# Optimization experiments

Measured on AMD Instinct MI355X. Metric: run time of the kernel, lower is better.

The kernel has to match this reference:

```python
import jax, jax.numpy as jnp
import numpy as np

N = 50000      # nodes
E = 800000     # edges
F_IN = 128     # infeatures
H = 64         # hidden_channels
NID = 1
MSG_EPS = 1e-7  # GENConv message eps


def layer_norm(x, g, b):
    mu = jnp.mean(x, axis=-1, keepdims=True)
    var = jnp.var(x, axis=-1, keepdims=True)
    return (x - mu) * jax.lax.rsqrt(var + 1e-5) * g + b


def gen_conv(x, src, dst, t, W1, b1, g1, be1, W2, b2):
    # message: relu(x_j) + eps, gathered along edges
    m = jax.nn.relu(x[src]) + MSG_EPS                      # [E, C]
    # softmax aggregation over incoming edges per destination node, per channel
    logits = m * t                                         # [E, C]
    seg_max = jax.ops.segment_max(logits, dst, num_segments=N)
    seg_max = jnp.where(jnp.isfinite(seg_max), seg_max, 0.0)  # isolated nodes
    ex = jnp.exp(logits - seg_max[dst])                    # [E, C]
    denom = jax.ops.segment_sum(ex, dst, num_segments=N)   # [N, C]
    alpha = ex / (denom[dst] + 1e-16)                      # softmax weights per edge
    agg = jax.ops.segment_sum(m * alpha, dst, num_segments=N)  # [N, C]
    out = agg + x                                          # add root
    # MLP: Linear(C->2C) -> LayerNorm -> ReLU -> Linear(2C->C)
    h = jax.nn.relu(layer_norm(out @ W1 + b1, g1, be1))
    return h @ W2 + b2


def setup_inputs() -> dict:
    key = jax.random.key(0)
    ks = jax.random.split(key, 12)
    s = 0.05
    return {
        "x": jax.random.normal(ks[0], (N, F_IN), dtype=jnp.float32),
        "edge_index": jax.random.randint(ks[1], (2, E), 0, N, dtype=jnp.int64),
        "enc_W": jax.random.normal(ks[2], (F_IN, H), dtype=jnp.float32) * s,
        "enc_b": jnp.zeros((H,), jnp.float32),
        "t": jnp.float32(1.0),
        "conv_W1": jax.random.normal(ks[3], (H, 2 * H), dtype=jnp.float32) * s,
        "conv_b1": jnp.zeros((2 * H,), jnp.float32),
        "conv_g1": jnp.ones((2 * H,), jnp.float32),
        "conv_be1": jnp.zeros((2 * H,), jnp.float32),
        "conv_W2": jax.random.normal(ks[4], (2 * H, H), dtype=jnp.float32) * s,
        "conv_b2": jnp.zeros((H,), jnp.float32),
        "ln1_g": jnp.ones((H,), jnp.float32),
        "ln1_b": jnp.zeros((H,), jnp.float32),
        "norm_g": jnp.ones((2 * H,), jnp.float32),
        "norm_b": jnp.zeros((2 * H,), jnp.float32),
        "lin_W": jax.random.normal(ks[5], (2 * H, NID), dtype=jnp.float32) * s,
        "lin_b": jnp.zeros((NID,), jnp.float32),
    }


def reference(x, edge_index, enc_W, enc_b, t, conv_W1, conv_b1, conv_g1, conv_be1,
              conv_W2, conv_b2, ln1_g, ln1_b, norm_g, norm_b, lin_W, lin_b):
    src, dst = edge_index[0], edge_index[1]
    x = x @ enc_W + enc_b                                   # node encoder [N, H]
    # pre-applied conv (layers[0].conv called standalone in original forward)
    x = gen_conv(x, src, dst, t, conv_W1, conv_b1, conv_g1, conv_be1, conv_W2, conv_b2)
    # DeepGCNLayer block='dense' (same conv module, shared weights)
    h = gen_conv(x, src, dst, t, conv_W1, conv_b1, conv_g1, conv_be1, conv_W2, conv_b2)
    h = jax.nn.relu(layer_norm(h, ln1_g, ln1_b))
    x = jnp.concatenate([x, h], axis=-1)                    # [N, 2H] (dropout eval = identity)
    x = jax.nn.relu(layer_norm(x, norm_g, norm_b))
    return x @ lin_W + lin_b                                # [N, NID]
```

## Files before the change

kernel.cpp:

```cpp
#include <hip/hip_runtime.h>
#include <hip/hip_bf16.h>


#define NN 50000
#define EE 800000
#define FIN 128
#define HD 64
#define NBUCK 196
#define CAP 4608
#define EPB 2048
#define NBLK 391

typedef unsigned short u16;
typedef unsigned int u32;
using bf16x8 = __attribute__((ext_vector_type(8))) short;
using f32x4 = __attribute__((ext_vector_type(4))) float;

__device__ __forceinline__ float bf2f(u16 u) {
    u32 x = ((u32)u) << 16;
    float f;
    __builtin_memcpy(&f, &x, 4);
    return f;
}
__device__ __forceinline__ short f2bf(float f) {
    u32 u;
    __builtin_memcpy(&u, &f, 4);
    u32 r = (u + 0x7fffu + ((u >> 16) & 1u)) >> 16;
    return (short)r;
}

__global__ __launch_bounds__(256) void k_detect(const int* __restrict__ ei,
                                                int* __restrict__ flag,
                                                int* __restrict__ bcnt) {
    __shared__ int red[256];
    int t = threadIdx.x;
    int any = 0;
#pragma unroll
    for (int k = 0; k < 4; k++) any |= (ei[2 * (t * 4 + k) + 1] != 0) ? 1 : 0;
    red[t] = any;
    __syncthreads();
    for (int d = 128; d >= 1; d >>= 1) {
        if (t < d) red[t] |= red[t + d];
        __syncthreads();
    }
    if (t == 0) *flag = red[0];
    if (t < NBUCK) bcnt[t] = 0;
}

__global__ __launch_bounds__(256) void k_bucket_enc(
    const int* __restrict__ ei, const int* __restrict__ flag, int* __restrict__ bcnt,
    u32* __restrict__ barr, const float* __restrict__ x, const float* __restrict__ W,
    const float* __restrict__ b, u16* __restrict__ Abf) {
    __shared__ short wtE[64 * 136];
    int tid = threadIdx.x;
    if (blockIdx.x < NBLK) {
        __shared__ int hist[NBUCK];
        __shared__ int gbase[NBUCK];
        __shared__ int cur[NBUCK];
        for (int i = tid; i < NBUCK; i += 256) { hist[i] = 0; cur[i] = 0; }
        __syncthreads();
        int is32 = *flag;
        int e0 = blockIdx.x * EPB;
        u32 pk[8];
#pragma unroll
        for (int j = 0; j < 8; j++) {
            int e = e0 + j * 256 + tid;
            if (e < EE) {
                int s, d;
                if (is32) {
                    s = ei[e];
                    d = ei[EE + e];
                } else {
                    int2 sp = ((const int2*)ei)[e];
                    int2 dp = ((const int2*)ei)[EE + e];
                    s = sp.x;
                    d = dp.x;
                }
                pk[j] = (u32)s | ((u32)(d & 255) << 16) | ((u32)(d >> 8) << 24);
                atomicAdd(&hist[d >> 8], 1);
            } else {
                pk[j] = 0xFFFFFFFFu;
            }
        }
        __syncthreads();
        for (int i = tid; i < NBUCK; i += 256)
            if (hist[i] > 0) gbase[i] = atomicAdd(&bcnt[i], hist[i]);
        __syncthreads();
#pragma unroll
        for (int j = 0; j < 8; j++) {
            if (pk[j] != 0xFFFFFFFFu) {
                int bk = pk[j] >> 24;
                int pos = gbase[bk] + atomicAdd(&cur[bk], 1);
                if (pos < CAP) barr[(size_t)bk * CAP + pos] = pk[j] & 0x00FFFFFFu;
            }
        }
        return;
    }
    for (int i = tid; i < FIN * HD; i += 256) wtE[(i & 63) * 136 + (i >> 6)] = f2bf(W[i]);
    __syncthreads();

    int lane = tid & 63, wid = tid >> 6;
    int l16 = lane & 15, q = lane >> 4;
    int m0 = (int)(blockIdx.x - NBLK) * 64 + wid * 16;
    int mrow = m0 + l16;
    if (mrow >= NN) mrow = NN - 1;

    bf16x8 af[4];
#pragma unroll
    for (int c = 0; c < 4; c++) {
        const float4* p = (const float4*)(x + (size_t)mrow * FIN + c * 32 + q * 8);
        float4 p0 = p[0], p1 = p[1];
        af[c][0] = f2bf(p0.x); af[c][1] = f2bf(p0.y); af[c][2] = f2bf(p0.z); af[c][3] = f2bf(p0.w);
        af[c][4] = f2bf(p1.x); af[c][5] = f2bf(p1.y); af[c][6] = f2bf(p1.z); af[c][7] = f2bf(p1.w);
    }
    f32x4 acc[4];
#pragma unroll
    for (int u = 0; u < 4; u++) {
        f32x4 z = {0.f, 0.f, 0.f, 0.f};
#pragma unroll
        for (int c = 0; c < 4; c++) {
            bf16x8 wf = *(const bf16x8*)(const void*)&wtE[(u * 16 + l16) * 136 + c * 32 + q * 8];
            z = __builtin_amdgcn_mfma_f32_16x16x32_bf16(af[c], wf, z, 0, 0, 0);
        }
        acc[u] = z;
    }
#pragma unroll
    for (int u = 0; u < 4; u++) {
        int col = u * 16 + l16;
        float bc = b[col];
#pragma unroll
        for (int r = 0; r < 4; r++) {
            int node = m0 + q * 4 + r;
            if (node < NN) Abf[(size_t)node * HD + col] = (u16)f2bf(acc[u][r] + bc);
        }
    }
}

__global__ __launch_bounds__(256) void k_sort(const int* __restrict__ bcnt,
                                              const u32* __restrict__ barr,
                                              u16* __restrict__ eSrc,
                                              int* __restrict__ rowLo,
                                              int* __restrict__ deg) {
    __shared__ u32 pkL[CAP];
    __shared__ u16 outL[CAP];
    __shared__ int hist[256];
    __shared__ int excl[256];
    __shared__ int cur[256];
    int bk = blockIdx.x;
    int t = threadIdx.x;
    int cnt = bcnt[bk];
    if (cnt > CAP) cnt = CAP;
    const u32* bp = barr + (size_t)bk * CAP;
    for (int i = t; i < cnt; i += 256) pkL[i] = bp[i];
    hist[t] = 0;
    __syncthreads();
    for (int i = t; i < cnt; i += 256) atomicAdd(&hist[(pkL[i] >> 16) & 0xFF], 1);
    __syncthreads();
    int v = hist[t];
    excl[t] = v;
    __syncthreads();
#pragma unroll
    for (int d = 1; d < 256; d <<= 1) {
        int u = (t >= d) ? excl[t - d] : 0;
        __syncthreads();
        excl[t] += u;
        __syncthreads();
    }
    int ex = excl[t] - v;
    cur[t] = ex;
    int node = bk * 256 + t;
    if (node < NN) {
        rowLo[node] = bk * CAP + ex;
        deg[node] = v;
    }
    __syncthreads();
    for (int i = t; i < cnt; i += 256) {
        u32 pk = pkL[i];
        int pos = atomicAdd(&cur[(pk >> 16) & 0xFF], 1);
        outL[pos] = (u16)pk;
    }
    __syncthreads();
    int cnt2 = (cnt + 1) >> 1;
    u32* dst = (u32*)(void*)(eSrc + (size_t)bk * CAP);
    const u32* src = (const u32*)(const void*)outL;
    for (int i = t; i < cnt2; i += 256) dst[i] = src[i];
}

__global__ __launch_bounds__(256) void k_agg(const u16* __restrict__ Xbf,
                                             const float* __restrict__ Xfp,
                                             const int* __restrict__ rowLo,
                                             const int* __restrict__ deg,
                                             const u16* __restrict__ eSrc,
                                             const float* __restrict__ tptr,
                                             u16* __restrict__ OUTbf) {
    int t = threadIdx.x;
    int lane = t & 63, wid = t >> 6;
    int half = lane >> 5, cp = lane & 31;
    float tt = tptr[0];
    for (int n = blockIdx.x * 4 + wid; n < NN; n += gridDim.x * 4) {
        int s = rowLo[n];
        int e = s + deg[n];
        float self0, self1;
        if (Xfp) {
            float2 f2 = *(const float2*)(Xfp + (size_t)n * HD + 2 * cp);
            self0 = f2.x; self1 = f2.y;
        } else {
            u32 u = *(const u32*)(const void*)(Xbf + (size_t)n * HD + 2 * cp);
            self0 = bf2f((u16)u); self1 = bf2f((u16)(u >> 16));
        }
        float num0 = 0.f, den0 = 0.f, num1 = 0.f, den1 = 0.f;
        int base = s;
        for (; base + 16 <= e; base += 16) {
            int sv[8];
#pragma unroll
            for (int k = 0; k < 8; k++) sv[k] = eSrc[base + 2 * k + half];
            u32 uu[8];
#pragma unroll
            for (int k = 0; k < 8; k++)
                uu[k] = *(const u32*)(const void*)(Xbf + (size_t)sv[k] * HD + 2 * cp);
#pragma unroll
            for (int k = 0; k < 8; k++) {
                float m0 = fmaxf(bf2f((u16)uu[k]), 0.f) + 1e-7f;
                float m1 = fmaxf(bf2f((u16)(uu[k] >> 16)), 0.f) + 1e-7f;
                float p0 = __expf(m0 * tt);
                float p1 = __expf(m1 * tt);
                den0 += p0; num0 += m0 * p0;
                den1 += p1; num1 += m1 * p1;
            }
        }
        if (base + 8 <= e) {
            int sv[4];
#pragma unroll
            for (int k = 0; k < 4; k++) sv[k] = eSrc[base + 2 * k + half];
            u32 uu[4];
#pragma unroll
            for (int k = 0; k < 4; k++)
                uu[k] = *(const u32*)(const void*)(Xbf + (size_t)sv[k] * HD + 2 * cp);
#pragma unroll
            for (int k = 0; k < 4; k++) {
                float m0 = fmaxf(bf2f((u16)uu[k]), 0.f) + 1e-7f;
                float m1 = fmaxf(bf2f((u16)(uu[k] >> 16)), 0.f) + 1e-7f;
                float p0 = __expf(m0 * tt);
                float p1 = __expf(m1 * tt);
                den0 += p0; num0 += m0 * p0;
                den1 += p1; num1 += m1 * p1;
            }
            base += 8;
        }
        int i = base + half;
        for (; i + 2 < e; i += 4) {
            int sva = eSrc[i], svb = eSrc[i + 2];
            u32 ua = *(const u32*)(const void*)(Xbf + (size_t)sva * HD + 2 * cp);
            u32 ub = *(const u32*)(const void*)(Xbf + (size_t)svb * HD + 2 * cp);
            float m0a = fmaxf(bf2f((u16)ua), 0.f) + 1e-7f;
            float m1a = fmaxf(bf2f((u16)(ua >> 16)), 0.f) + 1e-7f;
            float m0b = fmaxf(bf2f((u16)ub), 0.f) + 1e-7f;
            float m1b = fmaxf(bf2f((u16)(ub >> 16)), 0.f) + 1e-7f;
            float p0a = __expf(m0a * tt), p1a = __expf(m1a * tt);
            float p0b = __expf(m0b * tt), p1b = __expf(m1b * tt);
            den0 += p0a + p0b; num0 += m0a * p0a + m0b * p0b;
            den1 += p1a + p1b; num1 += m1a * p1a + m1b * p1b;
        }
        if (i < e) {
            int sv = eSrc[i];
            u32 u = *(const u32*)(const void*)(Xbf + (size_t)sv * HD + 2 * cp);
            float m0 = fmaxf(bf2f((u16)u), 0.f) + 1e-7f;
            float m1 = fmaxf(bf2f((u16)(u >> 16)), 0.f) + 1e-7f;
            float p0 = __expf(m0 * tt);
            float p1 = __expf(m1 * tt);
            den0 += p0; num0 += m0 * p0;
            den1 += p1; num1 += m1 * p1;
        }
        num0 += __shfl_xor(num0, 32, 64);
        den0 += __shfl_xor(den0, 32, 64);
        num1 += __shfl_xor(num1, 32, 64);
        den1 += __shfl_xor(den1, 32, 64);
        if (half == 0) {
            float a0 = num0 / (den0 + 1e-16f) + self0;
            float a1 = num1 / (den1 + 1e-16f) + self1;
            u32 pk = (u32)(u16)f2bf(a0) | ((u32)(u16)f2bf(a1) << 16);
            *(u32*)(void*)(OUTbf + (size_t)n * HD + 2 * cp) = pk;
        }
    }
}

__global__ __launch_bounds__(256) void k_mlp(const u16* __restrict__ INbf,
                                             const float* __restrict__ W1,
                                             const float* __restrict__ B1,
                                             const float* __restrict__ G1,
                                             const float* __restrict__ BE1,
                                             const float* __restrict__ W2,
                                             const float* __restrict__ B2,
                                             float* __restrict__ OUTfp,
                                             u16* __restrict__ OUTbf) {
    __shared__ short wt1[128 * 72];
    __shared__ short wt2[64 * 136];
    __shared__ short hbuf[64 * 136];
    int tid = threadIdx.x;
    for (int i = tid; i < HD * 128; i += 256) wt1[(i & 127) * 72 + (i >> 7)] = f2bf(W1[i]);
    for (int i = tid; i < 128 * HD; i += 256) wt2[(i & 63) * 136 + (i >> 6)] = f2bf(W2[i]);
    __syncthreads();

    int lane = tid & 63, wid = tid >> 6;
    int l16 = lane & 15, q = lane >> 4;
    int m0 = blockIdx.x * 64 + wid * 16;
    int mrow = m0 + l16;
    if (mrow >= NN) mrow = NN - 1;

    float b1v[8], g1v[8], bev[8];
#pragma unroll
    for (int tl = 0; tl < 8; tl++) {
        int j = tl * 16 + l16;
        b1v[tl] = B1[j]; g1v[tl] = G1[j]; bev[tl] = BE1[j];
    }

    bf16x8 a0 = *(const bf16x8*)(const void*)(INbf + (size_t)mrow * HD + q * 8);
    bf16x8 a1 = *(const bf16x8*)(const void*)(INbf + (size_t)mrow * HD + 32 + q * 8);
    f32x4 acc1[8];
#pragma unroll
    for (int tl = 0; tl < 8; tl++) {
        bf16x8 w0 = *(const bf16x8*)(const void*)&wt1[(tl * 16 + l16) * 72 + q * 8];
        bf16x8 w1 = *(const bf16x8*)(const void*)&wt1[(tl * 16 + l16) * 72 + 32 + q * 8];
        f32x4 z = {0.f, 0.f, 0.f, 0.f};
        z = __builtin_amdgcn_mfma_f32_16x16x32_bf16(a0, w0, z, 0, 0, 0);
        z = __builtin_amdgcn_mfma_f32_16x16x32_bf16(a1, w1, z, 0, 0, 0);
        acc1[tl] = z;
    }
    float S[4] = {0, 0, 0, 0}, Q[4] = {0, 0, 0, 0};
#pragma unroll
    for (int tl = 0; tl < 8; tl++)
#pragma unroll
        for (int r = 0; r < 4; r++) {
            float v = acc1[tl][r] + b1v[tl];
            acc1[tl][r] = v;
            S[r] += v; Q[r] += v * v;
        }
#pragma unroll
    for (int m = 8; m >= 1; m >>= 1)
#pragma unroll
        for (int r = 0; r < 4; r++) {
            S[r] += __shfl_xor(S[r], m, 64);
            Q[r] += __shfl_xor(Q[r], m, 64);
        }
    float mu[4], rs[4];
#pragma unroll
    for (int r = 0; r < 4; r++) {
        mu[r] = S[r] * (1.f / 128.f);
        float var = Q[r] * (1.f / 128.f) - mu[r] * mu[r];
        rs[r] = rsqrtf(var + 1e-5f);
    }
#pragma unroll
    for (int tl = 0; tl < 8; tl++)
#pragma unroll
        for (int r = 0; r < 4; r++) {
            float h = fmaxf((acc1[tl][r] - mu[r]) * rs[r] * g1v[tl] + bev[tl], 0.f);
            hbuf[(wid * 16 + q * 4 + r) * 136 + tl * 16 + l16] = f2bf(h);
        }

    bf16x8 a2[4];
#pragma unroll
    for (int c = 0; c < 4; c++)
        a2[c] = *(const bf16x8*)(const void*)&hbuf[(wid * 16 + l16) * 136 + c * 32 + q * 8];
    f32x4 acc2[4];
#pragma unroll
    for (int u = 0; u < 4; u++) {
        f32x4 z = {0.f, 0.f, 0.f, 0.f};
#pragma unroll
        for (int c = 0; c < 4; c++) {
            bf16x8 wf = *(const bf16x8*)(const void*)&wt2[(u * 16 + l16) * 136 + c * 32 + q * 8];
            z = __builtin_amdgcn_mfma_f32_16x16x32_bf16(a2[c], wf, z, 0, 0, 0);
        }
        acc2[u] = z;
    }
#pragma unroll
    for (int u = 0; u < 4; u++) {
        int col = u * 16 + l16;
        float bc = B2[col];
#pragma unroll
        for (int r = 0; r < 4; r++) {
            int node = m0 + q * 4 + r;
            if (node < NN) {
                float val = acc2[u][r] + bc;
                OUTfp[(size_t)node * HD + col] = val;
                OUTbf[(size_t)node * HD + col] = (u16)f2bf(val);
            }
        }
    }
}

__global__ __launch_bounds__(256) void k_mlpfin(const u16* __restrict__ INbf,
                                                const float* __restrict__ W1,
                                                const float* __restrict__ B1,
                                                const float* __restrict__ G1,
                                                const float* __restrict__ BE1,
                                                const float* __restrict__ W2,
                                                const float* __restrict__ B2,
                                                const float* __restrict__ X1,
                                                const float* __restrict__ LG,
                                                const float* __restrict__ LB,
                                                const float* __restrict__ NG,
                                                const float* __restrict__ NBv,
                                                const float* __restrict__ LW,
                                                const float* __restrict__ LBias,
                                                float* __restrict__ out) {
    __shared__ short wt1[128 * 72];
    __shared__ short wt2[64 * 136];
    __shared__ short hbuf[64 * 136];
    int tid = threadIdx.x;
    for (int i = tid; i < HD * 128; i += 256) wt1[(i & 127) * 72 + (i >> 7)] = f2bf(W1[i]);
    for (int i = tid; i < 128 * HD; i += 256) wt2[(i & 63) * 136 + (i >> 6)] = f2bf(W2[i]);
    __syncthreads();

    int lane = tid & 63, wid = tid >> 6;
    int l16 = lane & 15, q = lane >> 4;
    int m0 = blockIdx.x * 64 + wid * 16;
    int mrow = m0 + l16;
    if (mrow >= NN) mrow = NN - 1;

    float b1v[8], g1v[8], bev[8];
#pragma unroll
    for (int tl = 0; tl < 8; tl++) {
        int j = tl * 16 + l16;
        b1v[tl] = B1[j]; g1v[tl] = G1[j]; bev[tl] = BE1[j];
    }

    bf16x8 a0 = *(const bf16x8*)(const void*)(INbf + (size_t)mrow * HD + q * 8);
    bf16x8 a1 = *(const bf16x8*)(const void*)(INbf + (size_t)mrow * HD + 32 + q * 8);
    f32x4 acc1[8];
#pragma unroll
    for (int tl = 0; tl < 8; tl++) {
        bf16x8 w0 = *(const bf16x8*)(const void*)&wt1[(tl * 16 + l16) * 72 + q * 8];
        bf16x8 w1 = *(const bf16x8*)(const void*)&wt1[(tl * 16 + l16) * 72 + 32 + q * 8];
        f32x4 z = {0.f, 0.f, 0.f, 0.f};
        z = __builtin_amdgcn_mfma_f32_16x16x32_bf16(a0, w0, z, 0, 0, 0);
        z = __builtin_amdgcn_mfma_f32_16x16x32_bf16(a1, w1, z, 0, 0, 0);
        acc1[tl] = z;
    }
    float S[4] = {0, 0, 0, 0}, Q[4] = {0, 0, 0, 0};
#pragma unroll
    for (int tl = 0; tl < 8; tl++)
#pragma unroll
        for (int r = 0; r < 4; r++) {
            float v = acc1[tl][r] + b1v[tl];
            acc1[tl][r] = v;
            S[r] += v; Q[r] += v * v;
        }
#pragma unroll
    for (int m = 8; m >= 1; m >>= 1)
#pragma unroll
        for (int r = 0; r < 4; r++) {
            S[r] += __shfl_xor(S[r], m, 64);
            Q[r] += __shfl_xor(Q[r], m, 64);
        }
#pragma unroll
    for (int r = 0; r < 4; r++) {
        float mu = S[r] * (1.f / 128.f);
        float var = Q[r] * (1.f / 128.f) - mu * mu;
        float rs = rsqrtf(var + 1e-5f);
        S[r] = mu; Q[r] = rs;
    }
#pragma unroll
    for (int tl = 0; tl < 8; tl++)
#pragma unroll
        for (int r = 0; r < 4; r++) {
            float h = fmaxf((acc1[tl][r] - S[r]) * Q[r] * g1v[tl] + bev[tl], 0.f);
            hbuf[(wid * 16 + q * 4 + r) * 136 + tl * 16 + l16] = f2bf(h);
        }

    bf16x8 a2[4];
#pragma unroll
    for (int c = 0; c < 4; c++)
        a2[c] = *(const bf16x8*)(const void*)&hbuf[(wid * 16 + l16) * 136 + c * 32 + q * 8];
    f32x4 acc2[4];
#pragma unroll
    for (int u = 0; u < 4; u++) {
        f32x4 z = {0.f, 0.f, 0.f, 0.f};
#pragma unroll
        for (int c = 0; c < 4; c++) {
            bf16x8 wf = *(const bf16x8*)(const void*)&wt2[(u * 16 + l16) * 136 + c * 32 + q * 8];
            z = __builtin_amdgcn_mfma_f32_16x16x32_bf16(a2[c], wf, z, 0, 0, 0);
        }
        acc2[u] = z;
    }

    float lg[4], lbv[4], ng1[4], nb1[4], ng2[4], nb2[4], lw1[4], lw2[4], b2c[4];
#pragma unroll
    for (int u = 0; u < 4; u++) {
        int col = u * 16 + l16;
        b2c[u] = B2[col];
        lg[u] = LG[col]; lbv[u] = LB[col];
        ng1[u] = NG[col]; nb1[u] = NBv[col];
        ng2[u] = NG[64 + col]; nb2[u] = NBv[64 + col];
        lw1[u] = LW[col]; lw2[u] = LW[64 + col];
    }
    float lbias0 = LBias[0];

    float h2[4][4];
    float Sh[4] = {0, 0, 0, 0}, Qh[4] = {0, 0, 0, 0};
#pragma unroll
    for (int u = 0; u < 4; u++)
#pragma unroll
        for (int r = 0; r < 4; r++) {
            float v = acc2[u][r] + b2c[u];
            h2[u][r] = v;
            Sh[r] += v; Qh[r] += v * v;
        }
#pragma unroll
    for (int m = 8; m >= 1; m >>= 1)
#pragma unroll
        for (int r = 0; r < 4; r++) {
            Sh[r] += __shfl_xor(Sh[r], m, 64);
            Qh[r] += __shfl_xor(Qh[r], m, 64);
        }
    float hn[4][4], x1v[4][4];
    float S2[4] = {0, 0, 0, 0}, Q2[4] = {0, 0, 0, 0};
#pragma unroll
    for (int r = 0; r < 4; r++) {
        float mu = Sh[r] * (1.f / 64.f);
        float var = Qh[r] * (1.f / 64.f) - mu * mu;
        float rs = rsqrtf(var + 1e-5f);
        int node = m0 + q * 4 + r;
        int nodeC = node < NN ? node : NN - 1;
#pragma unroll
        for (int u = 0; u < 4; u++) {
            float h = fmaxf((h2[u][r] - mu) * rs * lg[u] + lbv[u], 0.f);
            hn[u][r] = h;
            float xv = X1[(size_t)nodeC * HD + u * 16 + l16];
            x1v[u][r] = xv;
            S2[r] += xv + h;
            Q2[r] += xv * xv + h * h;
        }
    }
#pragma unroll
    for (int m = 8; m >= 1; m >>= 1)
#pragma unroll
        for (int r = 0; r < 4; r++) {
            S2[r] += __shfl_xor(S2[r], m, 64);
            Q2[r] += __shfl_xor(Q2[r], m, 64);
        }
    float contrib[4];
#pragma unroll
    for (int r = 0; r < 4; r++) {
        float mu2 = S2[r] * (1.f / 128.f);
        float var2 = Q2[r] * (1.f / 128.f) - mu2 * mu2;
        float rs2 = rsqrtf(var2 + 1e-5f);
        float c = 0.f;
#pragma unroll
        for (int u = 0; u < 4; u++) {
            float av = fmaxf((x1v[u][r] - mu2) * rs2 * ng1[u] + nb1[u], 0.f);
            float bv = fmaxf((hn[u][r] - mu2) * rs2 * ng2[u] + nb2[u], 0.f);
            c += av * lw1[u] + bv * lw2[u];
        }
        contrib[r] = c;
    }
#pragma unroll
    for (int m = 8; m >= 1; m >>= 1)
#pragma unroll
        for (int r = 0; r < 4; r++) contrib[r] += __shfl_xor(contrib[r], m, 64);
    if (l16 == 0) {
#pragma unroll
        for (int r = 0; r < 4; r++) {
            int node = m0 + q * 4 + r;
            if (node < NN) out[node] = contrib[r] + lbias0;
        }
    }
}

extern "C" void kernel_launch(void* const* d_in, const int* in_sizes, int n_in,
                              void* d_out, int out_size, void* d_ws, size_t ws_size,
                              hipStream_t stream) {
    const float* x = (const float*)d_in[0];
    const int* ei = (const int*)d_in[1];
    const float* encW = (const float*)d_in[2];
    const float* encB = (const float*)d_in[3];
    const float* tptr = (const float*)d_in[4];
    const float* cW1 = (const float*)d_in[5];
    const float* cB1 = (const float*)d_in[6];
    const float* cG1 = (const float*)d_in[7];
    const float* cBE1 = (const float*)d_in[8];
    const float* cW2 = (const float*)d_in[9];
    const float* cB2 = (const float*)d_in[10];
    const float* ln1g = (const float*)d_in[11];
    const float* ln1b = (const float*)d_in[12];
    const float* ng = (const float*)d_in[13];
    const float* nb = (const float*)d_in[14];
    const float* lw = (const float*)d_in[15];
    const float* lb = (const float*)d_in[16];

    char* w = (char*)d_ws;
    size_t off = 0;
    auto carve = [&](size_t bytes) {
        void* p = w + off;
        off += (bytes + 255) & ~(size_t)255;
        return p;
    };
    int* flag = (int*)carve(4);
    int* bcnt = (int*)carve(NBUCK * 4);
    u32* barr = (u32*)carve((size_t)NBUCK * CAP * 4);
    int* rowLo = (int*)carve((size_t)NN * 4);
    int* deg = (int*)carve((size_t)NN * 4);
    u16* eSrc = (u16*)carve((size_t)NBUCK * CAP * 2);
    u16* Abf = (u16*)carve((size_t)NN * HD * 2);
    u16* AGbf = (u16*)carve((size_t)NN * HD * 2);
    float* X1 = (float*)carve((size_t)NN * HD * 4);
    u16* X1bf = (u16*)carve((size_t)NN * HD * 2);

    k_detect<<<1, 256, 0, stream>>>(ei, flag, bcnt);

    const int GB = (NN + 63) / 64;
    k_bucket_enc<<<NBLK + GB, 256, 0, stream>>>(ei, flag, bcnt, barr, x, encW, encB, Abf);
    k_sort<<<NBUCK, 256, 0, stream>>>(bcnt, barr, eSrc, rowLo, deg);

    k_agg<<<2048, 256, 0, stream>>>(Abf, nullptr, rowLo, deg, eSrc, tptr, AGbf);
    k_mlp<<<GB, 256, 0, stream>>>(AGbf, cW1, cB1, cG1, cBE1, cW2, cB2, X1, X1bf);
    k_agg<<<2048, 256, 0, stream>>>(X1bf, X1, rowLo, deg, eSrc, tptr, AGbf);
    k_mlpfin<<<GB, 256, 0, stream>>>(AGbf, cW1, cB1, cG1, cBE1, cW2, cB2, X1,
                                     ln1g, ln1b, ng, nb, lw, lb, (float*)d_out);
}
```

Measured before the change: 220.7 us.

## Process two nodes per wavefront in aggregation and pack row offset with degree

The aggregation kernel now handles two destination nodes per wavefront (n and n+N/2) and interleaves their edge gathers, issuing up to 16 independent row loads at once to raise memory-level parallelism. The separate rowLo and deg arrays become one int2 array, so each node needs a single load. The second aggregation now takes the root term from the bf16 copy instead of the fp32 X1, which slightly changes precision. Register pressure rises from the doubled accumulators and index arrays, which may lower occupancy.

```diff
diff --git a/kernel.cpp b/kernel.cpp
--- a/kernel.cpp
+++ b/kernel.cpp
@@ -139,8 +139,7 @@
 __global__ __launch_bounds__(256) void k_sort(const int* __restrict__ bcnt,
                                               const u32* __restrict__ barr,
                                               u16* __restrict__ eSrc,
-                                              int* __restrict__ rowLo,
-                                              int* __restrict__ deg) {
+                                              int2* __restrict__ rowdeg) {
     __shared__ u32 pkL[CAP];
     __shared__ u16 outL[CAP];
     __shared__ int hist[256];
@@ -169,10 +168,7 @@
     int ex = excl[t] - v;
     cur[t] = ex;
     int node = bk * 256 + t;
-    if (node < NN) {
-        rowLo[node] = bk * CAP + ex;
-        deg[node] = v;
-    }
+    if (node < NN) rowdeg[node] = make_int2(bk * CAP + ex, v);
     __syncthreads();
     for (int i = t; i < cnt; i += 256) {
         u32 pk = pkL[i];
@@ -187,9 +183,7 @@
 }
 
 __global__ __launch_bounds__(256) void k_agg(const u16* __restrict__ Xbf,
-                                             const float* __restrict__ Xfp,
-                                             const int* __restrict__ rowLo,
-                                             const int* __restrict__ deg,
+                                             const int2* __restrict__ rowdeg,
                                              const u16* __restrict__ eSrc,
                                              const float* __restrict__ tptr,
                                              u16* __restrict__ OUTbf) {
@@ -197,89 +191,113 @@
     int lane = t & 63, wid = t >> 6;
     int half = lane >> 5, cp = lane & 31;
     float tt = tptr[0];
-    for (int n = blockIdx.x * 4 + wid; n < NN; n += gridDim.x * 4) {
-        int s = rowLo[n];
-        int e = s + deg[n];
-        float self0, self1;
-        if (Xfp) {
-            float2 f2 = *(const float2*)(Xfp + (size_t)n * HD + 2 * cp);
-            self0 = f2.x; self1 = f2.y;
-        } else {
-            u32 u = *(const u32*)(const void*)(Xbf + (size_t)n * HD + 2 * cp);
-            self0 = bf2f((u16)u); self1 = bf2f((u16)(u >> 16));
-        }
-        float num0 = 0.f, den0 = 0.f, num1 = 0.f, den1 = 0.f;
-        int base = s;
-        for (; base + 16 <= e; base += 16) {
+    const int HALF = NN / 2;
+
+    auto edge = [tt](u32 u, float& n0_, float& d0_, float& n1_, float& d1_) {
+        float m0 = fmaxf(bf2f((u16)u), 0.f) + 1e-7f;
+        float m1 = fmaxf(bf2f((u16)(u >> 16)), 0.f) + 1e-7f;
+        float p0 = __expf(m0 * tt);
+        float p1 = __expf(m1 * tt);
+        d0_ += p0; n0_ += m0 * p0;
+        d1_ += p1; n1_ += m1 * p1;
+    };
+
+    for (int p = blockIdx.x * 4 + wid; p < HALF; p += gridDim.x * 4) {
+        int n0 = p, n1 = p + HALF;
+        int2 rd0 = rowdeg[n0], rd1 = rowdeg[n1];
+        int b0 = rd0.x, e0 = rd0.x + rd0.y;
+        int b1 = rd1.x, e1 = rd1.x + rd1.y;
+        u32 su0 = *(const u32*)(const void*)(Xbf + (size_t)n0 * HD + 2 * cp);
+        u32 su1 = *(const u32*)(const void*)(Xbf + (size_t)n1 * HD + 2 * cp);
+        float nA0 = 0, dA0 = 0, nA1 = 0, dA1 = 0;
+        float nB0 = 0, dB0 = 0, nB1 = 0, dB1 = 0;
+
+        while (b0 + 16 <= e0 && b1 + 16 <= e1) {
+            int sv[16];
+#pragma unroll
+            for (int k = 0; k < 8; k++) sv[k] = eSrc[b0 + 2 * k + half];
+#pragma unroll
+            for (int k = 0; k < 8; k++) sv[8 + k] = eSrc[b1 + 2 * k + half];
+            u32 uu[16];
+#pragma unroll
+            for (int k = 0; k < 16; k++)
+                uu[k] = *(const u32*)(const void*)(Xbf + (size_t)sv[k] * HD + 2 * cp);
+#pragma unroll
+            for (int k = 0; k < 8; k++) edge(uu[k], nA0, dA0, nA1, dA1);
+#pragma unroll
+            for (int k = 0; k < 8; k++) edge(uu[8 + k], nB0, dB0, nB1, dB1);
+            b0 += 16; b1 += 16;
+        }
+        while (b0 + 8 <= e0 && b1 + 8 <= e1) {
             int sv[8];
 #pragma unroll
-            for (int k = 0; k < 8; k++) sv[k] = eSrc[base + 2 * k + half];
+            for (int k = 0; k < 4; k++) sv[k] = eSrc[b0 + 2 * k + half];
+#pragma unroll
+            for (int k = 0; k < 4; k++) sv[4 + k] = eSrc[b1 + 2 * k + half];
             u32 uu[8];
 #pragma unroll
             for (int k = 0; k < 8; k++)
                 uu[k] = *(const u32*)(const void*)(Xbf + (size_t)sv[k] * HD + 2 * cp);
 #pragma unroll
-            for (int k = 0; k < 8; k++) {
-                float m0 = fmaxf(bf2f((u16)uu[k]), 0.f) + 1e-7f;
-                float m1 = fmaxf(bf2f((u16)(uu[k] >> 16)), 0.f) + 1e-7f;
-                float p0 = __expf(m0 * tt);
-                float p1 = __expf(m1 * tt);
-                den0 += p0; num0 += m0 * p0;
-                den1 += p1; num1 += m1 * p1;
+            for (int k = 0; k < 4; k++) edge(uu[k], nA0, dA0, nA1, dA1);
+#pragma unroll
+            for (int k = 0; k < 4; k++) edge(uu[4 + k], nB0, dB0, nB1, dB1);
+            b0 += 8; b1 += 8;
+        }
+
+        auto finish = [&](int base, int end, float& N0, float& D0, float& N1, float& D1) {
+            for (; base + 16 <= end; base += 16) {
+                int sv[8];
+#pragma unroll
+                for (int k = 0; k < 8; k++) sv[k] = eSrc[base + 2 * k + half];
+                u32 uu[8];
+#pragma unroll
+                for (int k = 0; k < 8; k++)
+                    uu[k] = *(const u32*)(const void*)(Xbf + (size_t)sv[k] * HD + 2 * cp);
+#pragma unroll
+                for (int k = 0; k < 8; k++) edge(uu[k], N0, D0, N1, D1);
             }
-        }
-        if (base + 8 <= e) {
-            int sv[4];
-#pragma unroll
-            for (int k = 0; k < 4; k++) sv[k] = eSrc[base + 2 * k + half];
-            u32 uu[4];
-#pragma unroll
-            for (int k = 0; k < 4; k++)
-                uu[k] = *(const u32*)(const void*)(Xbf + (size_t)sv[k] * HD + 2 * cp);
-#pragma unroll
-            for (int k = 0; k < 4; k++) {
-                float m0 = fmaxf(bf2f((u16)uu[k]), 0.f) + 1e-7f;
-                float m1 = fmaxf(bf2f((u16)(uu[k] >> 16)), 0.f) + 1e-7f;
-                float p0 = __expf(m0 * tt);
-                float p1 = __expf(m1 * tt);
-                den0 += p0; num0 += m0 * p0;
-                den1 += p1; num1 += m1 * p1;
+            if (base + 8 <= end) {
+                int sv[4];
+#pragma unroll
+                for (int k = 0; k < 4; k++) sv[k] = eSrc[base + 2 * k + half];
+                u32 uu[4];
+#pragma unroll
+                for (int k = 0; k < 4; k++)
+                    uu[k] = *(const u32*)(const void*)(Xbf + (size_t)sv[k] * HD + 2 * cp);
+#pragma unroll
+                for (int k = 0; k < 4; k++) edge(uu[k], N0, D0, N1, D1);
+                base += 8;
             }
-            base += 8;
-        }
-        int i = base + half;
-        for (; i + 2 < e; i += 4) {
-            int sva = eSrc[i], svb = eSrc[i + 2];
-            u32 ua = *(const u32*)(const void*)(Xbf + (size_t)sva * HD + 2 * cp);
-            u32 ub = *(const u32*)(const void*)(Xbf + (size_t)svb * HD + 2 * cp);
-            float m0a = fmaxf(bf2f((u16)ua), 0.f) + 1e-7f;
-            float m1a = fmaxf(bf2f((u16)(ua >> 16)), 0.f) + 1e-7f;
-            float m0b = fmaxf(bf2f((u16)ub), 0.f) + 1e-7f;
-            float m1b = fmaxf(bf2f((u16)(ub >> 16)), 0.f) + 1e-7f;
-            float p0a = __expf(m0a * tt), p1a = __expf(m1a * tt);
-            float p0b = __expf(m0b * tt), p1b = __expf(m1b * tt);
-            den0 += p0a + p0b; num0 += m0a * p0a + m0b * p0b;
-            den1 += p1a + p1b; num1 += m1a * p1a + m1b * p1b;
-        }
-        if (i < e) {
-            int sv = eSrc[i];
-            u32 u = *(const u32*)(const void*)(Xbf + (size_t)sv * HD + 2 * cp);
-            float m0 = fmaxf(bf2f((u16)u), 0.f) + 1e-7f;
-            float m1 = fmaxf(bf2f((u16)(u >> 16)), 0.f) + 1e-7f;
-            float p0 = __expf(m0 * tt);
-            float p1 = __expf(m1 * tt);
-            den0 += p0; num0 += m0 * p0;
-            den1 += p1; num1 += m1 * p1;
-        }
-        num0 += __shfl_xor(num0, 32, 64);
-        den0 += __shfl_xor(den0, 32, 64);
-        num1 += __shfl_xor(num1, 32, 64);
-        den1 += __shfl_xor(den1, 32, 64);
+            int i = base + half;
+            for (; i + 2 < end; i += 4) {
+                int sva = eSrc[i], svb = eSrc[i + 2];
+                u32 ua = *(const u32*)(const void*)(Xbf + (size_t)sva * HD + 2 * cp);
+                u32 ub = *(const u32*)(const void*)(Xbf + (size_t)svb * HD + 2 * cp);
+                edge(ua, N0, D0, N1, D1);
+                edge(ub, N0, D0, N1, D1);
+            }
+            if (i < end) {
+                u32 u = *(const u32*)(const void*)(Xbf + (size_t)eSrc[i] * HD + 2 * cp);
+                edge(u, N0, D0, N1, D1);
+            }
+        };
+        finish(b0, e0, nA0, dA0, nA1, dA1);
+        finish(b1, e1, nB0, dB0, nB1, dB1);
+
+        nA0 += __shfl_xor(nA0, 32, 64); dA0 += __shfl_xor(dA0, 32, 64);
+        nA1 += __shfl_xor(nA1, 32, 64); dA1 += __shfl_xor(dA1, 32, 64);
+        nB0 += __shfl_xor(nB0, 32, 64); dB0 += __shfl_xor(dB0, 32, 64);
+        nB1 += __shfl_xor(nB1, 32, 64); dB1 += __shfl_xor(dB1, 32, 64);
         if (half == 0) {
-            float a0 = num0 / (den0 + 1e-16f) + self0;
-            float a1 = num1 / (den1 + 1e-16f) + self1;
-            u32 pk = (u32)(u16)f2bf(a0) | ((u32)(u16)f2bf(a1) << 16);
-            *(u32*)(void*)(OUTbf + (size_t)n * HD + 2 * cp) = pk;
+            float a0 = nA0 / (dA0 + 1e-16f) + bf2f((u16)su0);
+            float a1 = nA1 / (dA1 + 1e-16f) + bf2f((u16)(su0 >> 16));
+            *(u32*)(void*)(OUTbf + (size_t)n0 * HD + 2 * cp) =
+                (u32)(u16)f2bf(a0) | ((u32)(u16)f2bf(a1) << 16);
+            float c0 = nB0 / (dB0 + 1e-16f) + bf2f((u16)su1);
+            float c1 = nB1 / (dB1 + 1e-16f) + bf2f((u16)(su1 >> 16));
+            *(u32*)(void*)(OUTbf + (size_t)n1 * HD + 2 * cp) =
+                (u32)(u16)f2bf(c0) | ((u32)(u16)f2bf(c1) << 16);
         }
     }
 }
@@ -597,8 +615,7 @@
     int* flag = (int*)carve(4);
     int* bcnt = (int*)carve(NBUCK * 4);
     u32* barr = (u32*)carve((size_t)NBUCK * CAP * 4);
-    int* rowLo = (int*)carve((size_t)NN * 4);
-    int* deg = (int*)carve((size_t)NN * 4);
+    int2* rowdeg = (int2*)carve((size_t)NN * 8);
     u16* eSrc = (u16*)carve((size_t)NBUCK * CAP * 2);
     u16* Abf = (u16*)carve((size_t)NN * HD * 2);
     u16* AGbf = (u16*)carve((size_t)NN * HD * 2);
@@ -609,11 +626,11 @@
 
     const int GB = (NN + 63) / 64;
     k_bucket_enc<<<NBLK + GB, 256, 0, stream>>>(ei, flag, bcnt, barr, x, encW, encB, Abf);
-    k_sort<<<NBUCK, 256, 0, stream>>>(bcnt, barr, eSrc, rowLo, deg);
-
-    k_agg<<<2048, 256, 0, stream>>>(Abf, nullptr, rowLo, deg, eSrc, tptr, AGbf);
+    k_sort<<<NBUCK, 256, 0, stream>>>(bcnt, barr, eSrc, rowdeg);
+
+    k_agg<<<2048, 256, 0, stream>>>(Abf, rowdeg, eSrc, tptr, AGbf);
     k_mlp<<<GB, 256, 0, stream>>>(AGbf, cW1, cB1, cG1, cBE1, cW2, cB2, X1, X1bf);
-    k_agg<<<2048, 256, 0, stream>>>(X1bf, X1, rowLo, deg, eSrc, tptr, AGbf);
+    k_agg<<<2048, 256, 0, stream>>>(X1bf, rowdeg, eSrc, tptr, AGbf);
     k_mlpfin<<<GB, 256, 0, stream>>>(AGbf, cW1, cB1, cG1, cBE1, cW2, cB2, X1,
                                      ln1g, ln1b, ng, nb, lw, lb, (float*)d_out);
 }
```

New measurement: 224.3 us. About the same (+1.6%).
